# Kernel optimization log

Measured on AMD Instinct MI355X. Metric: run time of the kernel, lower is better.

## Reference

```python
import jax, jax.numpy as jnp
import numpy as np

ORIG_VOCAB = 128000
PRUNED_VOCAB = 32000
EMB_DIM = 768
BATCH, SEQ = 16, 4096


def setup_inputs() -> dict:
    key = jax.random.key(0)
    k1, k2, k3 = jax.random.split(key, 3)
    input_ids = jax.random.randint(k1, (BATCH, SEQ), 0, ORIG_VOCAB, dtype=jnp.int32)
    lookup_table = jax.random.randint(k2, (ORIG_VOCAB,), 0, PRUNED_VOCAB, dtype=jnp.int32)
    emb_weight = jax.random.normal(k3, (PRUNED_VOCAB, EMB_DIM), dtype=jnp.float32)
    return {"input_ids": input_ids, "lookup_table": lookup_table, "emb_weight": emb_weight}


def reference(input_ids, lookup_table, emb_weight):
    # Vectorized form of the per-token dict remap: combined_map lookup with
    # default 0 is a dense gather from lookup_table (unknown ids already map
    # in-range here), followed by clamp to [0, embedding_size-1].
    mapped = lookup_table[input_ids]                      # [B, S] int32
    mapped = jnp.clip(mapped, 0, emb_weight.shape[0] - 1)  # clamp as in original
    # Downstream model's first op: token embedding gather.
    return emb_weight[mapped]                              # [B, S, D]
```

## Files before the change

kernel.cpp:

```cpp
#include <hip/hip_runtime.h>


constexpr int EMB_DIM   = 768;
constexpr int ROW_F4    = EMB_DIM / 4;
constexpr int VOCAB     = 32000;

typedef float vfloat4 __attribute__((ext_vector_type(4)));

__device__ __forceinline__ void store_nt_wa(vfloat4* p, vfloat4 v) {
    asm volatile("global_store_dwordx4 %0, %1, off sc0 sc1 nt"
                 :: "v"(p), "v"(v) : "memory");
}

__global__ __launch_bounds__(256) void token_emb_gather(
    const int*     __restrict__ input_ids,
    const int*     __restrict__ lookup,
    const vfloat4* __restrict__ emb,
    vfloat4*       __restrict__ out,
    int ntok)
{
    int token = blockIdx.x * 4 + threadIdx.y;
    if (token >= ntok) return;

    int id = lookup[input_ids[token]];
    id = min(max(id, 0), VOCAB - 1);

    const vfloat4* __restrict__ src = emb + (size_t)id    * ROW_F4;
    vfloat4*       __restrict__ dst = out + (size_t)token * ROW_F4;

    int lane = threadIdx.x;

    vfloat4 v0 = src[lane];
    vfloat4 v1 = src[lane + 64];
    vfloat4 v2 = src[lane + 128];
    store_nt_wa(dst + lane,       v0);
    store_nt_wa(dst + lane + 64,  v1);
    store_nt_wa(dst + lane + 128, v2);
}

extern "C" void kernel_launch(void* const* d_in, const int* in_sizes, int n_in,
                              void* d_out, int out_size, void* d_ws, size_t ws_size,
                              hipStream_t stream)
{
    const int*     input_ids = (const int*)d_in[0];
    const int*     lookup    = (const int*)d_in[1];
    const vfloat4* emb       = (const vfloat4*)d_in[2];
    vfloat4*       out       = (vfloat4*)d_out;

    int ntok = in_sizes[0];

    dim3 block(64, 4);
    dim3 grid((ntok + 3) / 4);
    token_emb_gather<<<grid, block, 0, stream>>>(input_ids, lookup, emb, out, ntok);
}
```

Measured before the change: 63.06 us.

## Bucket-sort tokens by embedding row before gather to improve cache locality

Adds a counting-sort pipeline (histogram, single-block scan, atomic scatter) that groups tokens by their embedding row bucket, then gathers rows in sorted order and writes each to its original token position. The aim is better L2/MALL reuse of embedding rows and less scattered DRAM traffic on reads. In exchange it adds four extra kernel launches, atomics, workspace traffic and scattered output writes. If the workspace is too small it falls back to the plain gather.

```diff
diff --git a/kernel.cpp b/kernel.cpp
--- a/kernel.cpp
+++ b/kernel.cpp
@@ -1,9 +1,13 @@
 #include <hip/hip_runtime.h>
 
 
-constexpr int EMB_DIM   = 768;
-constexpr int ROW_F4    = EMB_DIM / 4;
-constexpr int VOCAB     = 32000;
+constexpr int EMB_DIM  = 768;
+constexpr int ROW_F4   = EMB_DIM / 4;
+constexpr int VOCAB    = 32000;
+constexpr int NTOK     = 16 * 4096;
+constexpr int BSHIFT   = 5;
+constexpr int NBUCKET  = VOCAB >> BSHIFT;
+constexpr int SCANSZ   = 1024;
 
 typedef float vfloat4 __attribute__((ext_vector_type(4)));
 
@@ -12,24 +16,93 @@
                  :: "v"(p), "v"(v) : "memory");
 }
 
-__global__ __launch_bounds__(256) void token_emb_gather(
-    const int*     __restrict__ input_ids,
-    const int*     __restrict__ lookup,
+
+__global__ __launch_bounds__(1024) void zero_hist(int* __restrict__ hist) {
+    hist[threadIdx.x] = 0;
+}
+
+__global__ __launch_bounds__(256) void map_hist(
+    const int* __restrict__ input_ids,
+    const int* __restrict__ lookup,
+    int* __restrict__ mapped,
+    int* __restrict__ hist, int ntok)
+{
+    int t = blockIdx.x * blockDim.x + threadIdx.x;
+    if (t >= ntok) return;
+    int id = lookup[input_ids[t]];
+    id = min(max(id, 0), VOCAB - 1);
+    mapped[t] = id;
+    atomicAdd(&hist[id >> BSHIFT], 1);
+}
+
+__global__ __launch_bounds__(1024) void scan_excl(int* __restrict__ hist) {
+    __shared__ int tmp[SCANSZ];
+    int i = threadIdx.x;
+    int v = hist[i];
+    tmp[i] = v;
+    __syncthreads();
+    for (int off = 1; off < SCANSZ; off <<= 1) {
+        int add = (i >= off) ? tmp[i - off] : 0;
+        __syncthreads();
+        tmp[i] += add;
+        __syncthreads();
+    }
+    hist[i] = tmp[i] - v;
+}
+
+__global__ __launch_bounds__(256) void scatter(
+    const int* __restrict__ mapped,
+    int* __restrict__ hist,
+    int* __restrict__ sortedTok,
+    int* __restrict__ sortedId, int ntok)
+{
+    int t = blockIdx.x * blockDim.x + threadIdx.x;
+    if (t >= ntok) return;
+    int id  = mapped[t];
+    int pos = atomicAdd(&hist[id >> BSHIFT], 1);
+    sortedTok[pos] = t;
+    sortedId[pos]  = id;
+}
+
+
+__global__ __launch_bounds__(256) void token_emb_gather_sorted(
+    const int*     __restrict__ sortedTok,
+    const int*     __restrict__ sortedId,
     const vfloat4* __restrict__ emb,
-    vfloat4*       __restrict__ out,
-    int ntok)
+    vfloat4*       __restrict__ out, int ntok)
 {
-    int token = blockIdx.x * 4 + threadIdx.y;
-    if (token >= ntok) return;
+    int k = blockIdx.x * 4 + threadIdx.y;
+    if (k >= ntok) return;
 
-    int id = lookup[input_ids[token]];
-    id = min(max(id, 0), VOCAB - 1);
+    int token = sortedTok[k];
+    int id    = sortedId[k];
 
     const vfloat4* __restrict__ src = emb + (size_t)id    * ROW_F4;
     vfloat4*       __restrict__ dst = out + (size_t)token * ROW_F4;
 
     int lane = threadIdx.x;
+    vfloat4 v0 = src[lane];
+    vfloat4 v1 = src[lane + 64];
+    vfloat4 v2 = src[lane + 128];
+    store_nt_wa(dst + lane,       v0);
+    store_nt_wa(dst + lane + 64,  v1);
+    store_nt_wa(dst + lane + 128, v2);
+}
 
+
+__global__ __launch_bounds__(256) void token_emb_gather_plain(
+    const int*     __restrict__ input_ids,
+    const int*     __restrict__ lookup,
+    const vfloat4* __restrict__ emb,
+    vfloat4*       __restrict__ out, int ntok)
+{
+    int token = blockIdx.x * 4 + threadIdx.y;
+    if (token >= ntok) return;
+    int id = lookup[input_ids[token]];
+    id = min(max(id, 0), VOCAB - 1);
+    const vfloat4* __restrict__ src = emb + (size_t)id    * ROW_F4;
+    vfloat4*       __restrict__ dst = out + (size_t)token * ROW_F4;
+    int lane = threadIdx.x;
     vfloat4 v0 = src[lane];
     vfloat4 v1 = src[lane + 64];
     vfloat4 v2 = src[lane + 128];
@@ -49,7 +122,25 @@
 
     int ntok = in_sizes[0];
 
-    dim3 block(64, 4);
-    dim3 grid((ntok + 3) / 4);
-    token_emb_gather<<<grid, block, 0, stream>>>(input_ids, lookup, emb, out, ntok);
+    size_t need = (size_t)(3 * ntok + SCANSZ) * sizeof(int);
+    dim3 gblock(64, 4);
+    dim3 ggrid((ntok + 3) / 4);
+
+    if (ws_size < need) {
+        token_emb_gather_plain<<<ggrid, gblock, 0, stream>>>(input_ids, lookup, emb, out, ntok);
+        return;
+    }
+
+    int* mapped    = (int*)d_ws;
+    int* sortedTok = mapped + ntok;
+    int* sortedId  = sortedTok + ntok;
+    int* hist      = sortedId + ntok;
+
+    int nthread_blocks = (ntok + 255) / 256;
+
+    zero_hist<<<1, SCANSZ, 0, stream>>>(hist);
+    map_hist<<<nthread_blocks, 256, 0, stream>>>(input_ids, lookup, mapped, hist, ntok);
+    scan_excl<<<1, SCANSZ, 0, stream>>>(hist);
+    scatter<<<nthread_blocks, 256, 0, stream>>>(mapped, hist, sortedTok, sortedId, ntok);
+    token_emb_gather_sorted<<<ggrid, gblock, 0, stream>>>(sortedTok, sortedId, emb, out, ntok);
 }
```

After: 99.83 us. 1.58x slower.
